# Kernel optimization log

Measured on AMD Instinct MI355X. Metric: run time of the kernel, lower is better.

The kernel has to match this reference:

```python
import jax, jax.numpy as jnp
import numpy as np

WS = 7   # window size
SS = 3   # shift size
NH = 8   # num heads


def _rel_pos_index(ws):
    coords = np.stack(np.meshgrid(np.arange(ws), np.arange(ws), indexing='ij')).reshape(2, -1)
    rel = (coords[:, :, None] - coords[:, None, :]).transpose(1, 2, 0)  # (N,N,2)
    rel[..., 0] += ws - 1
    rel[..., 1] += ws - 1
    rel[..., 0] *= 2 * ws - 1
    return rel.sum(-1)  # (N,N) int


def _shift_attn_mask(hp, wp, ws, ss):
    img = np.zeros((hp, wp), dtype=np.float32)
    sl = (slice(0, -ws), slice(-ws, -ss), slice(-ss, None))
    cnt = 0
    for hs in sl:
        for vs in sl:
            img[hs, vs] = cnt
            cnt += 1
    mw = img.reshape(hp // ws, ws, wp // ws, ws).transpose(0, 2, 1, 3).reshape(-1, ws * ws)
    diff = mw[:, None, :] - mw[:, :, None]  # (nW,N,N)
    return np.where(diff != 0, -100.0, 0.0).astype(np.float32)


def _window_partition(x, ws):
    b, h, w, c = x.shape
    x = x.reshape(b, h // ws, ws, w // ws, ws, c).transpose(0, 1, 3, 2, 4, 5)
    return x.reshape(-1, ws * ws, c)


def _window_reverse(win, h, w, ws, b):
    c = win.shape[-1]
    x = win.reshape(b, h // ws, w // ws, ws, ws, c).transpose(0, 1, 3, 2, 4, 5)
    return x.reshape(b, h, w, c)


def setup_inputs() -> dict:
    key = jax.random.key(0)
    ks = jax.random.split(key, 6)
    B, H, W, C = 16, 56, 56, 256
    return {
        'query': jax.random.normal(ks[0], (B, H * W, C), jnp.float32),
        'w_qkv': jax.random.normal(ks[1], (C, 3 * C), jnp.float32) * 0.02,
        'b_qkv': jax.random.normal(ks[2], (3 * C,), jnp.float32) * 0.02,
        'w_proj': jax.random.normal(ks[3], (C, C), jnp.float32) * 0.02,
        'b_proj': jax.random.normal(ks[4], (C,), jnp.float32) * 0.02,
        'rel_bias_table': jax.random.normal(ks[5], ((2 * WS - 1) ** 2, NH), jnp.float32) * 0.02,
        'height': H,
        'width': W,
    }


def reference(query, w_qkv, b_qkv, w_proj, b_proj, rel_bias_table, height, width):
    B, L, C = query.shape
    ws, ss, nh = WS, SS, NH
    hd = C // nh
    scale = hd ** -0.5
    x = query.reshape(B, height, width, C)

    pad_b = (ws - height % ws) % ws
    pad_r = (ws - width % ws) % ws
    x = jnp.pad(x, ((0, 0), (0, pad_b), (0, pad_r), (0, 0)))
    hp, wp = height + pad_b, width + pad_r

    # cyclic shift
    x = jnp.roll(x, (-ss, -ss), axis=(1, 2))
    attn_mask = jnp.asarray(_shift_attn_mask(hp, wp, ws, ss))  # (nW,N,N)

    win = _window_partition(x, ws)  # (B*nW, N, C)
    BW, N, _ = win.shape
    nW = (hp // ws) * (wp // ws)

    qkv = (win @ w_qkv + b_qkv).reshape(BW, N, 3, nh, hd).transpose(2, 0, 3, 1, 4)
    q, k, v = qkv[0], qkv[1], qkv[2]  # (BW, nh, N, hd)

    attn = jnp.einsum('bhnd,bhmd->bhnm', q * scale, k)  # (BW,nh,N,N)
    bias = rel_bias_table[_rel_pos_index(ws).reshape(-1)].reshape(N, N, nh).transpose(2, 0, 1)
    attn = attn + bias[None]
    attn = attn.reshape(B, nW, nh, N, N) + attn_mask[None, :, None]
    attn = jax.nn.softmax(attn.reshape(BW, nh, N, N), axis=-1)

    out = jnp.einsum('bhnm,bhmd->bhnd', attn, v).transpose(0, 2, 1, 3).reshape(BW, N, C)
    out = out @ w_proj + b_proj

    x = _window_reverse(out, hp, wp, ws, B)
    x = jnp.roll(x, (ss, ss), axis=(1, 2))
    x = x[:, :height, :width, :]
    return x.reshape(B, height * width, C)
```

## Files before the change

### kernel.cpp

```cpp
#include <hip/hip_runtime.h>


#define IMG 56
#define SCALE2 (0.17677669529663687f * 1.4426950408889634f)
#define LOG2E 1.4426950408889634f

typedef unsigned short u16;
typedef unsigned int u32;
typedef unsigned long long u64;
typedef __attribute__((ext_vector_type(8))) short short8;
typedef __attribute__((ext_vector_type(4))) float floatx4;

__device__ __forceinline__ float bflo(u32 u) { return __uint_as_float(u << 16); }
__device__ __forceinline__ u16 f2bf(float f) {
  u32 u = __float_as_uint(f);
  return (u16)((u + 0x7fffu + ((u >> 16) & 1u)) >> 16);
}
__device__ __forceinline__ u32 cvt2(float lo, float hi) {
  u32 r;
  __asm__("v_cvt_pk_bf16_f32 %0, %1, %2" : "=v"(r) : "v"(lo), "v"(hi));
  return r;
}
__device__ __forceinline__ u16 f2bf1(float f) { return (u16)cvt2(f, f); }
__device__ __forceinline__ short8 pack8(float4 lo, float4 hi) {
  union { u32 u[4]; short8 s; } r;
  r.u[0] = cvt2(lo.x, lo.y); r.u[1] = cvt2(lo.z, lo.w);
  r.u[2] = cvt2(hi.x, hi.y); r.u[3] = cvt2(hi.z, hi.w);
  return r.s;
}
__device__ __forceinline__ float fexp2(float x) {
  float r; __asm__("v_exp_f32 %0, %1" : "=v"(r) : "v"(x)); return r;
}
#define MFMA(a, b, c) __builtin_amdgcn_mfma_f32_16x16x32_bf16(a, b, c, 0, 0, 0)
#define FENCE_LGKM() __asm__ volatile("s_waitcnt lgkmcnt(0)" ::: "memory")

__device__ __forceinline__ int qk_off(int tok, int dim) {
  return tok * 32 + ((((dim >> 3) ^ ((tok >> 2) & 3)) << 3) | (dim & 7));
}
__device__ __forceinline__ int p_off(int tok, int col) {
  return tok * 64 + ((((col >> 3) ^ ((tok >> 2) & 3)) << 3) | (col & 7));
}
__device__ __forceinline__ int vt_off(int dim, int tok) {
  return 4096 + dim * 64 + ((((tok >> 3) ^ ((dim >> 2) & 3)) << 3) | (tok & 7));
}
__device__ __forceinline__ int xs_off(int row, int col) {
  return row * 256 + (col >> 6) * 64 + ((((col >> 3) & 7) ^ (row & 7)) << 3) +
         (col & 7);
}

__global__ __launch_bounds__(256) void convert_kernel(
    const float* __restrict__ w_qkv, const float* __restrict__ w_proj,
    const float* __restrict__ bias_table, u16* __restrict__ zpad,
    u16* __restrict__ Wtq, u16* __restrict__ Wtp, u16* __restrict__ biasM) {
  int t = blockIdx.x * 256 + threadIdx.x;
  if (t < 196608) {
    int n = t % 768, k = t / 768;
    Wtq[n * 256 + k] = f2bf(w_qkv[t]);
  } else if (t < 262144) {
    int u = t - 196608;
    int n = u & 255, k = u >> 8;
    Wtp[n * 256 + k] = f2bf(w_proj[u]);
  } else if (t < 262272) {
    zpad[t - 262144] = 0;
  } else if (t < 393344) {
    int idx = t - 262272;
    int type = idx >> 15;
    int r = idx & 32767;
    int h = r >> 12, mt = (r >> 10) & 3, quad = (r >> 8) & 3;
    int l15 = (r >> 4) & 15, nt = (r >> 2) & 3, reg = r & 3;
    int row = 16 * mt + 4 * quad + reg;
    int col = 16 * nt + l15;
    float v;
    if (col >= 49) v = -1e30f;
    else if (row >= 49) v = 0.f;
    else {
      int yn = row / 7, xn = row - yn * 7;
      int ym = col / 7, xm = col - ym * 7;
      v = bias_table[((yn - ym + 6) * 13 + (xn - xm + 6)) * 8 + h];
      int bndH = (type >> 1) & 1, bndV = type & 1;
      int rc = (bndH ? ((yn < 4) ? 1 : 2) : 0) * 3 + (bndV ? ((xn < 4) ? 1 : 2) : 0);
      int cc = (bndH ? ((ym < 4) ? 1 : 2) : 0) * 3 + (bndV ? ((xm < 4) ? 1 : 2) : 0);
      if (rc != cc) v -= 100.f;
    }
    biasM[idx] = f2bf(v * LOG2E);
  }
}

__global__ __launch_bounds__(256) void fused_msa(
    const float* __restrict__ query, const u16* __restrict__ Wtq,
    const u16* __restrict__ Wtp, const float* __restrict__ b_qkv,
    const float* __restrict__ b_proj, const u16* __restrict__ biasM,
    float* __restrict__ out) {
  __shared__ __align__(16) u16 Xs[64 * 256];
  __shared__ __align__(16) u16 wscr[4][6144];
  const int tid = threadIdx.x;
  const int lane = tid & 63, w = tid >> 6;
  const int l15 = lane & 15, quad = lane >> 4;
  const int winl = blockIdx.x;
  const int img = winl >> 6, wi = (winl >> 3) & 7, wj = winl & 7;
  const int type = ((wi == 7) ? 2 : 0) | ((wj == 7) ? 1 : 0);

  #pragma unroll
  for (int it = 0; it < 8; ++it) {
    int idx = it * 256 + tid;
    int row = idx >> 5, cg = idx & 31;
    int kt = cg >> 3, sp = cg & 7;
    short8 pk = {};
    if (row < 49) {
      int pr = row / 7, pc = row - pr * 7;
      int y = wi * 7 + pr + 3; if (y >= IMG) y -= IMG;
      int x = wj * 7 + pc + 3; if (x >= IMG) x -= IMG;
      const float* src =
          query + (((size_t)(img * 3136 + y * IMG + x)) << 8) + cg * 8;
      float4 v0 = reinterpret_cast<const float4*>(src)[0];
      float4 v1 = reinterpret_cast<const float4*>(src)[1];
      pk = pack8(v0, v1);
    }
    *reinterpret_cast<short8*>(
        &Xs[row * 256 + kt * 64 + ((sp ^ (row & 7)) * 8)]) = pk;
  }
  __syncthreads();

  u16* wb = wscr[w];
  const floatx4 z4 = {0.f, 0.f, 0.f, 0.f};
  uint2 okp[2][4][2];

  #pragma unroll
  for (int hh = 0; hh < 2; ++hh) {
    const int h = 2 * w + hh;
    #pragma unroll
    for (int mat = 0; mat < 3; ++mat) {
      const int nbase = mat * 256 + h * 32;
      const u16* wr0 = Wtq + (size_t)(nbase + l15) * 256 + quad * 8;
      const u16* wr1 = wr0 + 16 * 256;
      floatx4 acc[4][2];
      #pragma unroll
      for (int mt = 0; mt < 4; ++mt) { acc[mt][0] = z4; acc[mt][1] = z4; }
      short8 b0 = *reinterpret_cast<const short8*>(wr0);
      short8 b1 = *reinterpret_cast<const short8*>(wr1);
      #pragma unroll
      for (int ks2 = 0; ks2 < 8; ++ks2) {
        short8 n0, n1;
        if (ks2 < 7) {
          n0 = *reinterpret_cast<const short8*>(wr0 + (ks2 + 1) * 32);
          n1 = *reinterpret_cast<const short8*>(wr1 + (ks2 + 1) * 32);
        }
        const int kt = ks2 >> 1;
        short8 af[4];
        #pragma unroll
        for (int mt = 0; mt < 4; ++mt)
          af[mt] = *reinterpret_cast<const short8*>(
              &Xs[(16 * mt + l15) * 256 + kt * 64 +
                  ((((ks2 & 1) * 4 + quad) ^ (l15 & 7)) * 8)]);
        #pragma unroll
        for (int mt = 0; mt < 4; ++mt) {
          acc[mt][0] = MFMA(af[mt], b0, acc[mt][0]);
          acc[mt][1] = MFMA(af[mt], b1, acc[mt][1]);
        }
        if (ks2 < 7) { b0 = n0; b1 = n1; }
      }
      float b0s = b_qkv[nbase + l15], b1s = b_qkv[nbase + 16 + l15];
      if (mat < 2) {
        const int mb = mat * 2048;
        #pragma unroll
        for (int mt = 0; mt < 4; ++mt)
          #pragma unroll
          for (int nt = 0; nt < 2; ++nt) {
            float bb = nt ? b1s : b0s;
            #pragma unroll
            for (int reg = 0; reg < 4; ++reg)
              wb[mb + qk_off(16 * mt + 4 * quad + reg, 16 * nt + l15)] =
                  f2bf1(acc[mt][nt][reg] + bb);
          }
      } else {
        #pragma unroll
        for (int mt = 0; mt < 4; ++mt)
          #pragma unroll
          for (int nt = 0; nt < 2; ++nt) {
            float bb = nt ? b1s : b0s;
            uint2 pv;
            pv.x = cvt2(acc[mt][nt][0] + bb, acc[mt][nt][1] + bb);
            pv.y = cvt2(acc[mt][nt][2] + bb, acc[mt][nt][3] + bb);
            *reinterpret_cast<uint2*>(
                &wb[vt_off(16 * nt + l15, 16 * mt + 4 * quad)]) = pv;
          }
      }
    }
    const u16* bbm = biasM + ((((type << 3) + h) << 12) + (quad << 8) + (l15 << 4));
    short8 bf0[4], bf1[4];
    #pragma unroll
    for (int mt = 0; mt < 4; ++mt) {
      bf0[mt] = *reinterpret_cast<const short8*>(bbm + (mt << 10));
      bf1[mt] = *reinterpret_cast<const short8*>(bbm + (mt << 10) + 8);
    }
    FENCE_LGKM();
    short8 qf[4], kf[4];
    #pragma unroll
    for (int mt = 0; mt < 4; ++mt)
      qf[mt] = *reinterpret_cast<const short8*>(&wb[qk_off(16 * mt + l15, quad * 8)]);
    #pragma unroll
    for (int nt = 0; nt < 4; ++nt)
      kf[nt] = *reinterpret_cast<const short8*>(
          &wb[2048 + qk_off(16 * nt + l15, quad * 8)]);
    floatx4 sc[4][4];
    #pragma unroll
    for (int mt = 0; mt < 4; ++mt)
      #pragma unroll
      for (int nt = 0; nt < 4; ++nt) sc[mt][nt] = MFMA(qf[mt], kf[nt], z4);
    #pragma unroll
    for (int mt = 0; mt < 4; ++mt)
      #pragma unroll
      for (int nt = 0; nt < 4; ++nt)
        #pragma unroll
        for (int reg = 0; reg < 4; ++reg) {
          u16 bv = (nt < 2) ? (u16)bf0[mt][(nt << 2) | reg]
                            : (u16)bf1[mt][((nt & 1) << 2) | reg];
          sc[mt][nt][reg] = sc[mt][nt][reg] * SCALE2 + bflo((u32)bv);
        }
    float inv_s[4][4];
    #pragma unroll
    for (int mt = 0; mt < 4; ++mt)
      #pragma unroll
      for (int reg = 0; reg < 4; ++reg) {
        float sum = 0.f;
        #pragma unroll
        for (int nt = 0; nt < 4; ++nt) {
          float e = fexp2(sc[mt][nt][reg]);
          sc[mt][nt][reg] = e; sum += e;
        }
        sum += __shfl_xor(sum, 1); sum += __shfl_xor(sum, 2);
        sum += __shfl_xor(sum, 4); sum += __shfl_xor(sum, 8);
        inv_s[mt][reg] = 1.f / sum;
      }
    #pragma unroll
    for (int mt = 0; mt < 4; ++mt)
      #pragma unroll
      for (int nt = 0; nt < 4; ++nt)
        #pragma unroll
        for (int reg = 0; reg < 4; ++reg)
          wb[p_off(16 * mt + 4 * quad + reg, 16 * nt + l15)] =
              f2bf1(sc[mt][nt][reg]);
    FENCE_LGKM();
    floatx4 oa[4][2];
    #pragma unroll
    for (int mt = 0; mt < 4; ++mt) { oa[mt][0] = z4; oa[mt][1] = z4; }
    #pragma unroll
    for (int ks = 0; ks < 2; ++ks) {
      short8 pf[4], vf[2];
      #pragma unroll
      for (int mt = 0; mt < 4; ++mt)
        pf[mt] = *reinterpret_cast<const short8*>(
            &wb[p_off(16 * mt + l15, ks * 32 + quad * 8)]);
      #pragma unroll
      for (int ntl = 0; ntl < 2; ++ntl)
        vf[ntl] = *reinterpret_cast<const short8*>(
            &wb[vt_off(16 * ntl + l15, ks * 32 + quad * 8)]);
      #pragma unroll
      for (int mt = 0; mt < 4; ++mt)
        #pragma unroll
        for (int ntl = 0; ntl < 2; ++ntl)
          oa[mt][ntl] = MFMA(pf[mt], vf[ntl], oa[mt][ntl]);
    }
    #pragma unroll
    for (int mt = 0; mt < 4; ++mt)
      #pragma unroll
      for (int ntl = 0; ntl < 2; ++ntl) {
        okp[hh][mt][ntl].x = cvt2(oa[mt][ntl][0] * inv_s[mt][0],
                                  oa[mt][ntl][1] * inv_s[mt][1]);
        okp[hh][mt][ntl].y = cvt2(oa[mt][ntl][2] * inv_s[mt][2],
                                  oa[mt][ntl][3] * inv_s[mt][3]);
      }
    FENCE_LGKM();
  }
  __syncthreads();
  #pragma unroll
  for (int hh = 0; hh < 2; ++hh) {
    int h = 2 * w + hh;
    #pragma unroll
    for (int mt = 0; mt < 4; ++mt)
      #pragma unroll
      for (int ntl = 0; ntl < 2; ++ntl) {
        int r0 = 16 * mt + 4 * quad;
        int col = h * 32 + 16 * ntl + l15;
        u32 lo = okp[hh][mt][ntl].x, hi = okp[hh][mt][ntl].y;
        Xs[xs_off(r0 + 0, col)] = (u16)lo;
        Xs[xs_off(r0 + 1, col)] = (u16)(lo >> 16);
        Xs[xs_off(r0 + 2, col)] = (u16)hi;
        Xs[xs_off(r0 + 3, col)] = (u16)(hi >> 16);
      }
  }
  __syncthreads();
  floatx4 pacc[4][4];
  #pragma unroll
  for (int i = 0; i < 4; ++i)
    #pragma unroll
    for (int j = 0; j < 4; ++j) pacc[i][j] = z4;
  const u16* wpp[4];
  #pragma unroll
  for (int nt = 0; nt < 4; ++nt)
    wpp[nt] = Wtp + (size_t)(w * 64 + 16 * nt + l15) * 256 + quad * 8;
  short8 bc[4];
  #pragma unroll
  for (int nt = 0; nt < 4; ++nt)
    bc[nt] = *reinterpret_cast<const short8*>(wpp[nt]);
  #pragma unroll
  for (int ks2 = 0; ks2 < 8; ++ks2) {
    short8 bn[4];
    if (ks2 < 7) {
      #pragma unroll
      for (int nt = 0; nt < 4; ++nt)
        bn[nt] = *reinterpret_cast<const short8*>(wpp[nt] + (ks2 + 1) * 32);
    }
    const int kt = ks2 >> 1;
    short8 af[4];
    #pragma unroll
    for (int mt = 0; mt < 4; ++mt)
      af[mt] = *reinterpret_cast<const short8*>(
          &Xs[(16 * mt + l15) * 256 + kt * 64 +
              ((((ks2 & 1) * 4 + quad) ^ (l15 & 7)) * 8)]);
    #pragma unroll
    for (int mt = 0; mt < 4; ++mt)
      #pragma unroll
      for (int nt = 0; nt < 4; ++nt)
        pacc[mt][nt] = MFMA(af[mt], bc[nt], pacc[mt][nt]);
    if (ks2 < 7) {
      #pragma unroll
      for (int nt = 0; nt < 4; ++nt) bc[nt] = bn[nt];
    }
  }
  float bp[4];
  #pragma unroll
  for (int nt = 0; nt < 4; ++nt) bp[nt] = b_proj[w * 64 + 16 * nt + l15];
  #pragma unroll
  for (int mt = 0; mt < 4; ++mt)
    #pragma unroll
    for (int reg = 0; reg < 4; ++reg) {
      int tokr = 16 * mt + 4 * quad + reg;
      if (tokr < 49) {
        int pr = tokr / 7, pc = tokr - pr * 7;
        int y = wi * 7 + pr + 3; if (y >= IMG) y -= IMG;
        int x = wj * 7 + pc + 3; if (x >= IMG) x -= IMG;
        float* op = out + (((size_t)(img * 3136 + y * IMG + x)) << 8) + w * 64;
        #pragma unroll
        for (int nt = 0; nt < 4; ++nt)
          op[16 * nt + l15] = pacc[mt][nt][reg] + bp[nt];
      }
    }
}

extern "C" void kernel_launch(void* const* d_in, const int* in_sizes, int n_in,
                              void* d_out, int out_size, void* d_ws, size_t ws_size,
                              hipStream_t stream) {
  const float* query      = (const float*)d_in[0];
  const float* w_qkv      = (const float*)d_in[1];
  const float* b_qkv      = (const float*)d_in[2];
  const float* w_proj     = (const float*)d_in[3];
  const float* b_proj     = (const float*)d_in[4];
  const float* bias_table = (const float*)d_in[5];

  u16* wsu   = (u16*)d_ws;
  u16* zpad  = wsu;
  u16* Wtq   = wsu + 128;
  u16* Wtp   = wsu + 196736;
  u16* biasM = wsu + 262272;

  convert_kernel<<<1537, 256, 0, stream>>>(w_qkv, w_proj, bias_table,
                                           zpad, Wtq, Wtp, biasM);
  fused_msa<<<1024, 256, 0, stream>>>(query, Wtq, Wtp, b_qkv, b_proj, biasM,
                                      (float*)d_out);
}
```

Measured before the change: 224.1 us.

## Transpose score MFMA to K-major, row-pack P stores, drop manual weight prefetch

Computes scores as K^T·Q so each lane holds a full query row across registers. This makes the softmax row sum two cross-half shuffles instead of four, and lets normalized P be written as packed 8-byte stores rather than scalar 2-byte stores. The bias-matrix layout and LDS swizzles are changed to match, and normalization moves before the PV MFMA. It also removes the manual register double-buffering of global weight loads in the QKV and proj GEMMs, leaving load scheduling to the compiler, which may expose load latency.

```diff
diff --git a/kernel.cpp b/kernel.cpp
--- a/kernel.cpp
+++ b/kernel.cpp
@@ -35,13 +35,13 @@
 #define FENCE_LGKM() __asm__ volatile("s_waitcnt lgkmcnt(0)" ::: "memory")
 
 __device__ __forceinline__ int qk_off(int tok, int dim) {
-  return tok * 32 + ((((dim >> 3) ^ ((tok >> 2) & 3)) << 3) | (dim & 7));
-}
-__device__ __forceinline__ int p_off(int tok, int col) {
-  return tok * 64 + ((((col >> 3) ^ ((tok >> 2) & 3)) << 3) | (col & 7));
+  return tok * 32 + ((((dim >> 3) ^ ((tok >> 1) & 3)) << 3) | (dim & 7));
+}
+__device__ __forceinline__ int p_off(int q, int k) {
+  return q * 64 + ((((k >> 3) ^ (q & 7)) << 3) | (k & 7));
 }
 __device__ __forceinline__ int vt_off(int dim, int tok) {
-  return 4096 + dim * 64 + ((((tok >> 3) ^ ((dim >> 2) & 3)) << 3) | (tok & 7));
+  return 4096 + dim * 64 + ((((tok >> 3) ^ (dim & 7)) << 3) | (tok & 7));
 }
 __device__ __forceinline__ int xs_off(int row, int col) {
   return row * 256 + (col >> 6) * 64 + ((((col >> 3) & 7) ^ (row & 7)) << 3) +
@@ -68,14 +68,14 @@
     int r = idx & 32767;
     int h = r >> 12, mt = (r >> 10) & 3, quad = (r >> 8) & 3;
     int l15 = (r >> 4) & 15, nt = (r >> 2) & 3, reg = r & 3;
-    int row = 16 * mt + 4 * quad + reg;
-    int col = 16 * nt + l15;
+    int q = 16 * mt + l15;
+    int k = 16 * nt + 4 * quad + reg;
     float v;
-    if (col >= 49) v = -1e30f;
-    else if (row >= 49) v = 0.f;
+    if (k >= 49) v = -1e30f;
+    else if (q >= 49) v = 0.f;
     else {
-      int yn = row / 7, xn = row - yn * 7;
-      int ym = col / 7, xm = col - ym * 7;
+      int yn = q / 7, xn = q - yn * 7;
+      int ym = k / 7, xm = k - ym * 7;
       v = bias_table[((yn - ym + 6) * 13 + (xn - xm + 6)) * 8 + h];
       int bndH = (type >> 1) & 1, bndV = type & 1;
       int rc = (bndH ? ((yn < 4) ? 1 : 2) : 0) * 3 + (bndV ? ((xn < 4) ? 1 : 2) : 0);
@@ -136,15 +136,10 @@
       floatx4 acc[4][2];
       #pragma unroll
       for (int mt = 0; mt < 4; ++mt) { acc[mt][0] = z4; acc[mt][1] = z4; }
-      short8 b0 = *reinterpret_cast<const short8*>(wr0);
-      short8 b1 = *reinterpret_cast<const short8*>(wr1);
       #pragma unroll
       for (int ks2 = 0; ks2 < 8; ++ks2) {
-        short8 n0, n1;
-        if (ks2 < 7) {
-          n0 = *reinterpret_cast<const short8*>(wr0 + (ks2 + 1) * 32);
-          n1 = *reinterpret_cast<const short8*>(wr1 + (ks2 + 1) * 32);
-        }
+        short8 b0 = *reinterpret_cast<const short8*>(wr0 + ks2 * 32);
+        short8 b1 = *reinterpret_cast<const short8*>(wr1 + ks2 * 32);
         const int kt = ks2 >> 1;
         short8 af[4];
         #pragma unroll
@@ -157,7 +152,6 @@
           acc[mt][0] = MFMA(af[mt], b0, acc[mt][0]);
           acc[mt][1] = MFMA(af[mt], b1, acc[mt][1]);
         }
-        if (ks2 < 7) { b0 = n0; b1 = n1; }
       }
       float b0s = b_qkv[nbase + l15], b1s = b_qkv[nbase + 16 + l15];
       if (mat < 2) {
@@ -206,7 +200,7 @@
     #pragma unroll
     for (int mt = 0; mt < 4; ++mt)
       #pragma unroll
-      for (int nt = 0; nt < 4; ++nt) sc[mt][nt] = MFMA(qf[mt], kf[nt], z4);
+      for (int nt = 0; nt < 4; ++nt) sc[mt][nt] = MFMA(kf[nt], qf[mt], z4);
     #pragma unroll
     for (int mt = 0; mt < 4; ++mt)
       #pragma unroll
@@ -217,29 +211,32 @@
                             : (u16)bf1[mt][((nt & 1) << 2) | reg];
           sc[mt][nt][reg] = sc[mt][nt][reg] * SCALE2 + bflo((u32)bv);
         }
-    float inv_s[4][4];
-    #pragma unroll
-    for (int mt = 0; mt < 4; ++mt)
-      #pragma unroll
-      for (int reg = 0; reg < 4; ++reg) {
-        float sum = 0.f;
-        #pragma unroll
-        for (int nt = 0; nt < 4; ++nt) {
+    float inv_s[4];
+    #pragma unroll
+    for (int mt = 0; mt < 4; ++mt) {
+      float sum = 0.f;
+      #pragma unroll
+      for (int nt = 0; nt < 4; ++nt)
+        #pragma unroll
+        for (int reg = 0; reg < 4; ++reg) {
           float e = fexp2(sc[mt][nt][reg]);
           sc[mt][nt][reg] = e; sum += e;
         }
-        sum += __shfl_xor(sum, 1); sum += __shfl_xor(sum, 2);
-        sum += __shfl_xor(sum, 4); sum += __shfl_xor(sum, 8);
-        inv_s[mt][reg] = 1.f / sum;
-      }
-    #pragma unroll
-    for (int mt = 0; mt < 4; ++mt)
-      #pragma unroll
-      for (int nt = 0; nt < 4; ++nt)
-        #pragma unroll
-        for (int reg = 0; reg < 4; ++reg)
-          wb[p_off(16 * mt + 4 * quad + reg, 16 * nt + l15)] =
-              f2bf1(sc[mt][nt][reg]);
+      sum += __shfl_xor(sum, 16); sum += __shfl_xor(sum, 32);
+      inv_s[mt] = 1.f / sum;
+    }
+    #pragma unroll
+    for (int mt = 0; mt < 4; ++mt) {
+      float iv = inv_s[mt];
+      #pragma unroll
+      for (int nt = 0; nt < 4; ++nt) {
+        uint2 pv;
+        pv.x = cvt2(sc[mt][nt][0] * iv, sc[mt][nt][1] * iv);
+        pv.y = cvt2(sc[mt][nt][2] * iv, sc[mt][nt][3] * iv);
+        *reinterpret_cast<uint2*>(
+            &wb[p_off(16 * mt + l15, 16 * nt + 4 * quad)]) = pv;
+      }
+    }
     FENCE_LGKM();
     floatx4 oa[4][2];
     #pragma unroll
@@ -265,10 +262,8 @@
     for (int mt = 0; mt < 4; ++mt)
       #pragma unroll
       for (int ntl = 0; ntl < 2; ++ntl) {
-        okp[hh][mt][ntl].x = cvt2(oa[mt][ntl][0] * inv_s[mt][0],
-                                  oa[mt][ntl][1] * inv_s[mt][1]);
-        okp[hh][mt][ntl].y = cvt2(oa[mt][ntl][2] * inv_s[mt][2],
-                                  oa[mt][ntl][3] * inv_s[mt][3]);
+        okp[hh][mt][ntl].x = cvt2(oa[mt][ntl][0], oa[mt][ntl][1]);
+        okp[hh][mt][ntl].y = cvt2(oa[mt][ntl][2], oa[mt][ntl][3]);
       }
     FENCE_LGKM();
   }
@@ -295,24 +290,14 @@
   for (int i = 0; i < 4; ++i)
     #pragma unroll
     for (int j = 0; j < 4; ++j) pacc[i][j] = z4;
-  const u16* wpp[4];
-  #pragma unroll
-  for (int nt = 0; nt < 4; ++nt)
-    wpp[nt] = Wtp + (size_t)(w * 64 + 16 * nt + l15) * 256 + quad * 8;
-  short8 bc[4];
-  #pragma unroll
-  for (int nt = 0; nt < 4; ++nt)
-    bc[nt] = *reinterpret_cast<const short8*>(wpp[nt]);
   #pragma unroll
   for (int ks2 = 0; ks2 < 8; ++ks2) {
-    short8 bn[4];
-    if (ks2 < 7) {
-      #pragma unroll
-      for (int nt = 0; nt < 4; ++nt)
-        bn[nt] = *reinterpret_cast<const short8*>(wpp[nt] + (ks2 + 1) * 32);
-    }
     const int kt = ks2 >> 1;
-    short8 af[4];
+    short8 af[4], bfp[4];
+    #pragma unroll
+    for (int nt = 0; nt < 4; ++nt)
+      bfp[nt] = *reinterpret_cast<const short8*>(
+          Wtp + (size_t)(w * 64 + 16 * nt + l15) * 256 + ks2 * 32 + quad * 8);
     #pragma unroll
     for (int mt = 0; mt < 4; ++mt)
       af[mt] = *reinterpret_cast<const short8*>(
@@ -322,11 +307,7 @@
     for (int mt = 0; mt < 4; ++mt)
       #pragma unroll
       for (int nt = 0; nt < 4; ++nt)
-        pacc[mt][nt] = MFMA(af[mt], bc[nt], pacc[mt][nt]);
-    if (ks2 < 7) {
-      #pragma unroll
-      for (int nt = 0; nt < 4; ++nt) bc[nt] = bn[nt];
-    }
+        pacc[mt][nt] = MFMA(af[mt], bfp[nt], pacc[mt][nt]);
   }
   float bp[4];
   #pragma unroll
```

After: 182.0 us. -18.8%, faster.
